# Kernel optimization log

Measured on AMD Instinct MI355X. Metric: run time of the kernel, lower is better.

Reference implementation:

```python
import jax, jax.numpy as jnp
import numpy as np

B, N, C, H = 1, 4096, 512, 8
S = 64  # sqrt(N), static


def setup_inputs() -> dict:
    key = jax.random.key(0)
    ks = jax.random.split(key, 4)
    d = C // H
    return {
        "x": jax.random.normal(ks[0], (B, N, C), dtype=jnp.float32),
        "num_heads": H,
        "bias": jnp.zeros((1,), dtype=jnp.float32),  # unused in original forward
        "scale": jnp.asarray(d ** -0.5, dtype=jnp.float32),
        "Wqkv": jax.random.normal(ks[1], (3 * C, C), dtype=jnp.float32) * (C ** -0.5),
        "bqkv": jnp.zeros((3 * C,), dtype=jnp.float32),
        "Wproj": jax.random.normal(ks[2], (C, C), dtype=jnp.float32) * (C ** -0.5),
        "bproj": jnp.zeros((C,), dtype=jnp.float32),
    }


def reference(x, num_heads, bias, scale, Wqkv, bqkv, Wproj, bproj):
    b, n, c = x.shape
    d = c // num_heads
    # fused QKV projection: [b, n, 3c] -> [3, b, h, n, d]
    qkv = (x @ Wqkv.T + bqkv).reshape(b, n, 3, num_heads, d).transpose(2, 0, 3, 1, 4)
    q, k, v = qkv[0] * scale, qkv[1], qkv[2]
    attn = jax.nn.softmax(jnp.einsum("bhnd,bhmd->bhnm", q, k), axis=-1)
    out = jnp.einsum("bhnm,bhmd->bhnd", attn, v)
    out = out.transpose(0, 2, 1, 3).reshape(b, n, c)
    out = out @ Wproj.T + bproj
    return out.reshape(b, S, S, c)
```

## Files before the change

### kernel.cpp

```cpp
#include <hip/hip_runtime.h>
#include <stdint.h>

#define NTOK 4096
#define CDIM 512
#define HEADS 8
#define DHEAD 64
#define PHEAD (NTOK * DHEAD)

typedef __bf16 bf16x8 __attribute__((ext_vector_type(8)));
typedef float f32x4 __attribute__((ext_vector_type(4)));

typedef const __attribute__((address_space(1))) unsigned int* gas_ptr;
typedef __attribute__((address_space(3))) unsigned int* las_ptr;

__device__ __forceinline__ unsigned short bfbits(float f) {
    return __builtin_bit_cast(unsigned short, (__bf16)f);
}

__device__ __forceinline__ f32x4 mfma32(bf16x8 a, bf16x8 b, f32x4 c) {
    return __builtin_amdgcn_mfma_f32_16x16x32_bf16(a, b, c, 0, 0, 0);
}

__device__ __forceinline__ void gload16(const unsigned short* g, unsigned short* l) {
    __builtin_amdgcn_global_load_lds((gas_ptr)g, (las_ptr)l, 16, 0, 0);
}

__device__ __forceinline__ void cvt_store8(unsigned short* dst, float4 v0, float4 v1) {
    unsigned short o[8];
    o[0] = bfbits(v0.x); o[1] = bfbits(v0.y); o[2] = bfbits(v0.z); o[3] = bfbits(v0.w);
    o[4] = bfbits(v1.x); o[5] = bfbits(v1.y); o[6] = bfbits(v1.z); o[7] = bfbits(v1.w);
    *(uint4*)dst = *(const uint4*)o;
}

__global__ __launch_bounds__(256) void cast3_k(
    const float* __restrict__ x, const float* __restrict__ wq, const float* __restrict__ wp,
    unsigned short* __restrict__ xb, unsigned short* __restrict__ wqb,
    unsigned short* __restrict__ wpb)
{
    const int b = blockIdx.x;
    const float* src; unsigned short* dst; int off;
    if (b < 1024)      { src = x;  dst = xb;  off = b; }
    else if (b < 1408) { src = wq; dst = wqb; off = b - 1024; }
    else               { src = wp; dst = wpb; off = b - 1408; }
    const int i = (off * 256 + threadIdx.x) * 8;
    const float4 v0 = *(const float4*)(src + i);
    const float4 v1 = *(const float4*)(src + i + 4);
    cvt_store8(dst + i, v0, v1);
}

__global__ __launch_bounds__(256) void gemm_qkv(
    const unsigned short* __restrict__ A,
    const unsigned short* __restrict__ Bm,
    const float* __restrict__ bias,
    const float* __restrict__ scale_p,
    unsigned short* __restrict__ qkv_out)
{
    __shared__ __align__(16) unsigned short smem[2 * 6144];

    const int tid = threadIdx.x;
    const int mBase = blockIdx.y * 64, nBase = blockIdx.x * 128;
    const int lane = tid & 63;
    const int w = __builtin_amdgcn_readfirstlane(tid >> 6);
    const int l16 = lane & 15, quad = lane >> 4;

    const int srow = tid >> 2;
    const int scol = ((tid & 3) ^ ((tid >> 3) & 3)) * 8;
    const unsigned short* gA  = &A[(size_t)(mBase + srow) * CDIM + scol];
    const unsigned short* gB0 = &Bm[(size_t)(nBase + srow) * CDIM + scol];
    const unsigned short* gB1 = &Bm[(size_t)(nBase + 64 + srow) * CDIM + scol];

    const int qs = (quad ^ ((l16 >> 1) & 3)) * 8;

    f32x4 acc[4][2] = {};

    gload16(gA, &smem[tid * 8]);
    gload16(gB0, &smem[2048 + tid * 8]);
    gload16(gB1, &smem[4096 + tid * 8]);

    int cur = 0;
    for (int kt = 0; kt < CDIM; kt += 32) {
        __syncthreads();
        if (kt + 32 < CDIM) {
            const int nb = (cur ^ 1) * 6144;
            gload16(gA + kt + 32, &smem[nb + tid * 8]);
            gload16(gB0 + kt + 32, &smem[nb + 2048 + tid * 8]);
            gload16(gB1 + kt + 32, &smem[nb + 4096 + tid * 8]);
        }
        const unsigned short* lA = &smem[cur * 6144];
        const unsigned short* lB = &smem[cur * 6144 + 2048];

        bf16x8 af[4], bfr[2];
#pragma unroll
        for (int i = 0; i < 4; ++i)
            af[i] = *(const bf16x8*)&lA[(i * 16 + l16) * 32 + qs];
#pragma unroll
        for (int j = 0; j < 2; ++j)
            bfr[j] = *(const bf16x8*)&lB[(w * 32 + j * 16 + l16) * 32 + qs];
#pragma unroll
        for (int i = 0; i < 4; ++i)
#pragma unroll
            for (int j = 0; j < 2; ++j)
                acc[i][j] = mfma32(af[i], bfr[j], acc[i][j]);
        cur ^= 1;
    }

    const int three = nBase >> 9;
    const float scl = scale_p[0] * 1.44269504f;
    const float mul = (three == 0) ? scl : 1.0f;

    __syncthreads();
#pragma unroll
    for (int i = 0; i < 4; ++i)
#pragma unroll
        for (int j = 0; j < 2; ++j)
#pragma unroll
            for (int r = 0; r < 4; ++r) {
                const int rl = i * 16 + quad * 4 + r;
                const int cl = w * 32 + j * 16 + l16;
                const float v = (acc[i][j][r] + bias[nBase + cl]) * mul;
                smem[rl * 136 + cl] = bfbits(v);
            }
    __syncthreads();

    const size_t base3 = (size_t)three * (PHEAD * HEADS);
    if (three < 2) {
#pragma unroll
        for (int pass = 0; pass < 4; ++pass) {
            const int idx = pass * 256 + tid;
            const int rl16 = idx & 15, qc = (idx >> 4) & 7;
            const int hsel = (idx >> 7) & 1, t16l = (idx >> 8) & 3;
            const uint4 d = *(const uint4*)&smem[(t16l * 16 + rl16) * 136 + hsel * 64 + qc * 8];
            const int hh = ((nBase >> 6) + hsel) & 7;
            const int t16 = (mBase >> 4) + t16l;
            const size_t dst = base3 + (size_t)hh * PHEAD +
                (size_t)(((t16 * 2 + (qc >> 2)) * 64 + (qc & 3) * 16 + rl16) * 8);
            *(uint4*)&qkv_out[dst] = d;
        }
    } else {
#pragma unroll
        for (int pass = 0; pass < 4; ++pass) {
            const int idx = pass * 256 + tid;
            const int l16t = idx & 15, quadt = (idx >> 4) & 3;
            const int dt = (idx >> 6) & 3, k32l = (idx >> 8) & 1, hsel = (idx >> 9) & 1;
            const int col = hsel * 64 + dt * 16 + l16t;
            unsigned short o8[8];
#pragma unroll
            for (int e = 0; e < 4; ++e) {
                o8[e]     = smem[(k32l * 32 + quadt * 4 + e) * 136 + col];
                o8[e + 4] = smem[(k32l * 32 + 16 + quadt * 4 + e) * 136 + col];
            }
            const int hh = ((nBase >> 6) + hsel) & 7;
            const int k32 = (mBase >> 5) + k32l;
            const size_t dst = base3 + (size_t)hh * PHEAD +
                (size_t)(((k32 * 4 + dt) * 64 + quadt * 16 + l16t) * 8);
            *(uint4*)&qkv_out[dst] = *(uint4*)o8;
        }
    }
}

__global__ __launch_bounds__(256, 2) void flash8_k(
    const unsigned short* __restrict__ qf,
    const unsigned short* __restrict__ kf,
    const unsigned short* __restrict__ vf,
    unsigned short* __restrict__ attn_out)
{
    __shared__ float ldsO[4][64][68];
    __shared__ float sml[4][64];

    const int tid = threadIdx.x;
    const int lane = tid & 63;
    const int w = __builtin_amdgcn_readfirstlane(tid >> 6);
    const int l16 = lane & 15, quad = lane >> 4;
    const int h = blockIdx.x, qb = blockIdx.y;

    const unsigned short* qh = qf + (size_t)h * PHEAD;
    const unsigned short* kb = kf + (size_t)h * PHEAD + w * 65536;
    const unsigned short* vb = vf + (size_t)h * PHEAD + w * 65536;

    bf16x8 qfr[4][2];
#pragma unroll
    for (int qt = 0; qt < 4; ++qt)
#pragma unroll
        for (int d2 = 0; d2 < 2; ++d2)
            qfr[qt][d2] = *(const bf16x8*)&qh[((qb * 4 + qt) * 2 + d2) * 512 + lane * 8];

    f32x4 oacc[4][4] = {};
    float lv[4] = {};

    bf16x8 kA[4], kB[4], vA[4], vB[4];
#pragma unroll
    for (int i = 0; i < 4; ++i) {
        kA[i] = *(const bf16x8*)&kb[i * 512 + lane * 8];
        vA[i] = *(const bf16x8*)&vb[i * 512 + lane * 8];
    }

    auto body = [&](int g, bf16x8* kuse, bf16x8* kload, bf16x8* vuse, bf16x8* vload) {
        const int gn = (g + 1) & 31;
#pragma unroll
        for (int i = 0; i < 4; ++i)
            kload[i] = *(const bf16x8*)&kb[gn * 2048 + i * 512 + lane * 8];
#pragma unroll
        for (int i = 0; i < 4; ++i)
            vload[i] = *(const bf16x8*)&vb[gn * 2048 + i * 512 + lane * 8];

        f32x4 s0[4], s1[4];
        __builtin_amdgcn_s_setprio(1);
#pragma unroll
        for (int qt = 0; qt < 4; ++qt) {
            f32x4 a = {};
            a = mfma32(kuse[0], qfr[qt][0], a);
            a = mfma32(kuse[1], qfr[qt][1], a);
            s0[qt] = a;
            f32x4 b = {};
            b = mfma32(kuse[2], qfr[qt][0], b);
            b = mfma32(kuse[3], qfr[qt][1], b);
            s1[qt] = b;
        }
        __builtin_amdgcn_s_setprio(0);

        bf16x8 pf[4];
#pragma unroll
        for (int qt = 0; qt < 4; ++qt) {
            float e0[4], e1[4];
#pragma unroll
            for (int r = 0; r < 4; ++r) {
                e0[r] = __builtin_amdgcn_exp2f(s0[qt][r]);
                e1[r] = __builtin_amdgcn_exp2f(s1[qt][r]);
            }
            lv[qt] += ((e0[0] + e0[1]) + (e0[2] + e0[3])) +
                      ((e1[0] + e1[1]) + (e1[2] + e1[3]));
            bf16x8 pb;
#pragma unroll
            for (int r = 0; r < 4; ++r) {
                pb[r]     = (__bf16)e0[r];
                pb[4 + r] = (__bf16)e1[r];
            }
            pf[qt] = pb;
        }

        __builtin_amdgcn_s_setprio(1);
#pragma unroll
        for (int dt = 0; dt < 4; ++dt)
#pragma unroll
            for (int qt = 0; qt < 4; ++qt)
                oacc[dt][qt] = mfma32(vuse[dt], pf[qt], oacc[dt][qt]);
        __builtin_amdgcn_s_setprio(0);
    };

    for (int it = 0; it < 16; ++it) {
        body(it * 2 + 0, kA, kB, vA, vB);
        body(it * 2 + 1, kB, kA, vB, vA);
    }

#pragma unroll
    for (int qt = 0; qt < 4; ++qt) {
        float L = lv[qt];
        L += __shfl_xor(L, 16, 64);
        L += __shfl_xor(L, 32, 64);
        if (quad == 0) sml[w][qt * 16 + l16] = L;
    }
#pragma unroll
    for (int qt = 0; qt < 4; ++qt) {
        const int q = qt * 16 + l16;
#pragma unroll
        for (int dt = 0; dt < 4; ++dt)
            *(f32x4*)&ldsO[w][q][dt * 16 + quad * 4] = oacc[dt][qt];
    }
    __syncthreads();
#pragma unroll
    for (int pass = 0; pass < 2; ++pass) {
        const int idx = pass * 256 + tid;
        const int q = idx >> 3, dseg = (idx & 7) * 8;
        const float L = sml[0][q] + sml[1][q] + sml[2][q] + sml[3][q];
        const float inv = 1.f / L;
        unsigned short o8[8];
#pragma unroll
        for (int i = 0; i < 8; ++i) {
            const float v = ldsO[0][q][dseg + i] + ldsO[1][q][dseg + i] +
                            ldsO[2][q][dseg + i] + ldsO[3][q][dseg + i];
            o8[i] = bfbits(v * inv);
        }
        *(uint4*)&attn_out[(size_t)(qb * 64 + q) * CDIM + h * DHEAD + dseg] = *(uint4*)o8;
    }
}

__global__ __launch_bounds__(256) void gemm_proj(
    const unsigned short* __restrict__ A,
    const unsigned short* __restrict__ Bm,
    const float* __restrict__ bias,
    float* __restrict__ c_out)
{
    __shared__ __align__(16) unsigned short smem[2 * 4096];

    const int tid = threadIdx.x;
    const int mBase = blockIdx.y * 64, nBase = blockIdx.x * 64;
    const int lane = tid & 63;
    const int w = __builtin_amdgcn_readfirstlane(tid >> 6);
    const int l16 = lane & 15, quad = lane >> 4;

    const int srow = tid >> 2;
    const int scol = ((tid & 3) ^ ((tid >> 3) & 3)) * 8;
    const unsigned short* gA = &A[(size_t)(mBase + srow) * CDIM + scol];
    const unsigned short* gB = &Bm[(size_t)(nBase + srow) * CDIM + scol];

    const int qs = (quad ^ ((l16 >> 1) & 3)) * 8;

    f32x4 acc[4] = {};

    gload16(gA, &smem[tid * 8]);
    gload16(gB, &smem[2048 + tid * 8]);

    int cur = 0;
    for (int kt = 0; kt < CDIM; kt += 32) {
        __syncthreads();
        if (kt + 32 < CDIM) {
            const int nb = (cur ^ 1) * 4096;
            gload16(gA + kt + 32, &smem[nb + tid * 8]);
            gload16(gB + kt + 32, &smem[nb + 2048 + tid * 8]);
        }
        const unsigned short* lA = &smem[cur * 4096];
        const unsigned short* lB = &smem[cur * 4096 + 2048];

        bf16x8 af[4], bfr;
#pragma unroll
        for (int i = 0; i < 4; ++i)
            af[i] = *(const bf16x8*)&lA[(i * 16 + l16) * 32 + qs];
        bfr = *(const bf16x8*)&lB[(w * 16 + l16) * 32 + qs];
#pragma unroll
        for (int i = 0; i < 4; ++i)
            acc[i] = mfma32(af[i], bfr, acc[i]);
        cur ^= 1;
    }

#pragma unroll
    for (int i = 0; i < 4; ++i)
#pragma unroll
        for (int r = 0; r < 4; ++r) {
            const int grow = mBase + i * 16 + quad * 4 + r;
            const int gcol = nBase + w * 16 + l16;
            c_out[(size_t)grow * CDIM + gcol] = acc[i][r] + bias[gcol];
        }
}

extern "C" void kernel_launch(void* const* d_in, const int* in_sizes, int n_in,
                              void* d_out, int out_size, void* d_ws, size_t ws_size,
                              hipStream_t stream) {
    const float* x       = (const float*)d_in[0];
    const float* scale_p = (const float*)d_in[3];
    const float* Wqkv    = (const float*)d_in[4];
    const float* bqkv    = (const float*)d_in[5];
    const float* Wproj   = (const float*)d_in[6];
    const float* bproj   = (const float*)d_in[7];
    float* out = (float*)d_out;

    char* ws = (char*)d_ws;
    const size_t OFF_QKV  = 0;
    const size_t OFF_ATTN = 12582912;
    const size_t OFF_XB   = 16777216;
    const size_t OFF_WQB  = 20971520;
    const size_t OFF_WPB  = 22544384;
    const size_t NEEDED   = OFF_WPB + 524288;
    if (ws_size < NEEDED) return;

    unsigned short* qkvb  = (unsigned short*)(ws + OFF_QKV);
    unsigned short* attnb = (unsigned short*)(ws + OFF_ATTN);
    unsigned short* xb    = (unsigned short*)(ws + OFF_XB);
    unsigned short* wqb   = (unsigned short*)(ws + OFF_WQB);
    unsigned short* wpb   = (unsigned short*)(ws + OFF_WPB);

    cast3_k<<<1536, 256, 0, stream>>>(x, Wqkv, Wproj, xb, wqb, wpb);

    gemm_qkv<<<dim3(12, 64), 256, 0, stream>>>(xb, wqb, bqkv, scale_p, qkvb);

    const unsigned short* qfr = qkvb;
    const unsigned short* kfr = qkvb + (size_t)PHEAD * HEADS;
    const unsigned short* vfr = qkvb + (size_t)2 * PHEAD * HEADS;
    flash8_k<<<dim3(8, 64), 256, 0, stream>>>(qfr, kfr, vfr, attnb);

    gemm_proj<<<dim3(8, 64), 256, 0, stream>>>(attnb, wpb, bproj, out);
}
```

Baseline: 131.4 us.

## Stage K/V tiles through LDS with async global-to-LDS double buffering

The attention kernel stops prefetching K and V into register double buffers and instead copies each tile into a double-buffered LDS region with global_load_lds. Each iteration then reads its fragments back from LDS, with a block barrier per iteration. The output-reduction epilogue now reuses the same 64KB buffer and works in two 32-row halves so everything fits. The aim is to lower register pressure and let the async copies hide load latency, at the cost of a barrier every iteration and extra LDS traffic.

Result: slower. 137.0 us (+4.2%).

```diff
diff --git a/kernel.cpp b/kernel.cpp
--- a/kernel.cpp
+++ b/kernel.cpp
@@ -158,14 +158,13 @@
     }
 }
 
-__global__ __launch_bounds__(256, 2) void flash8_k(
+__global__ __launch_bounds__(256, 2) void flash13_k(
     const unsigned short* __restrict__ qf,
     const unsigned short* __restrict__ kf,
     const unsigned short* __restrict__ vf,
     unsigned short* __restrict__ attn_out)
 {
-    __shared__ float ldsO[4][64][68];
-    __shared__ float sml[4][64];
+    __shared__ __align__(16) char sbuf[65536];
 
     const int tid = threadIdx.x;
     const int lane = tid & 63;
@@ -187,33 +186,40 @@
     f32x4 oacc[4][4] = {};
     float lv[4] = {};
 
-    bf16x8 kA[4], kB[4], vA[4], vB[4];
-#pragma unroll
-    for (int i = 0; i < 4; ++i) {
-        kA[i] = *(const bf16x8*)&kb[i * 512 + lane * 8];
-        vA[i] = *(const bf16x8*)&vb[i * 512 + lane * 8];
-    }
-
-    auto body = [&](int g, bf16x8* kuse, bf16x8* kload, bf16x8* vuse, bf16x8* vload) {
-        const int gn = (g + 1) & 31;
-#pragma unroll
-        for (int i = 0; i < 4; ++i)
-            kload[i] = *(const bf16x8*)&kb[gn * 2048 + i * 512 + lane * 8];
-#pragma unroll
-        for (int i = 0; i < 4; ++i)
-            vload[i] = *(const bf16x8*)&vb[gn * 2048 + i * 512 + lane * 8];
+    unsigned short* stg = (unsigned short*)sbuf + w * 4096;
+
+    auto STAGE = [&](int b, int g) {
+        unsigned short* s = stg + b * 16384;
+#pragma unroll
+        for (int i = 0; i < 4; ++i) {
+            gload16(&kb[g * 2048 + i * 512 + lane * 8], &s[i * 512 + lane * 8]);
+            gload16(&vb[g * 2048 + i * 512 + lane * 8], &s[2048 + i * 512 + lane * 8]);
+        }
+    };
+
+    STAGE(0, 0);
+    int cur = 0;
+    for (int g = 0; g < 32; ++g) {
+        __syncthreads();
+        if (g + 1 < 32) STAGE(cur ^ 1, g + 1);
+        const unsigned short* s = stg + cur * 16384;
+
+        bf16x8 kk[4];
+#pragma unroll
+        for (int i = 0; i < 4; ++i)
+            kk[i] = *(const bf16x8*)&s[i * 512 + lane * 8];
 
         f32x4 s0[4], s1[4];
         __builtin_amdgcn_s_setprio(1);
 #pragma unroll
         for (int qt = 0; qt < 4; ++qt) {
             f32x4 a = {};
-            a = mfma32(kuse[0], qfr[qt][0], a);
-            a = mfma32(kuse[1], qfr[qt][1], a);
+            a = mfma32(kk[0], qfr[qt][0], a);
+            a = mfma32(kk[1], qfr[qt][1], a);
             s0[qt] = a;
             f32x4 b = {};
-            b = mfma32(kuse[2], qfr[qt][0], b);
-            b = mfma32(kuse[3], qfr[qt][1], b);
+            b = mfma32(kk[2], qfr[qt][0], b);
+            b = mfma32(kk[3], qfr[qt][1], b);
             s1[qt] = b;
         }
         __builtin_amdgcn_s_setprio(0);
@@ -238,19 +244,25 @@
             pf[qt] = pb;
         }
 
+        bf16x8 vv[4];
+#pragma unroll
+        for (int i = 0; i < 4; ++i)
+            vv[i] = *(const bf16x8*)&s[2048 + i * 512 + lane * 8];
+
         __builtin_amdgcn_s_setprio(1);
 #pragma unroll
         for (int dt = 0; dt < 4; ++dt)
 #pragma unroll
             for (int qt = 0; qt < 4; ++qt)
-                oacc[dt][qt] = mfma32(vuse[dt], pf[qt], oacc[dt][qt]);
+                oacc[dt][qt] = mfma32(vv[dt], pf[qt], oacc[dt][qt]);
         __builtin_amdgcn_s_setprio(0);
-    };
-
-    for (int it = 0; it < 16; ++it) {
-        body(it * 2 + 0, kA, kB, vA, vB);
-        body(it * 2 + 1, kB, kA, vB, vA);
-    }
+        cur ^= 1;
+    }
+
+    __syncthreads();
+
+    float (*ldsO)[32][68] = (float(*)[32][68])sbuf;
+    float (*sml)[64]      = (float(*)[64])(sbuf + 34816);
 
 #pragma unroll
     for (int qt = 0; qt < 4; ++qt) {
@@ -259,28 +271,33 @@
         L += __shfl_xor(L, 32, 64);
         if (quad == 0) sml[w][qt * 16 + l16] = L;
     }
-#pragma unroll
-    for (int qt = 0; qt < 4; ++qt) {
-        const int q = qt * 16 + l16;
-#pragma unroll
-        for (int dt = 0; dt < 4; ++dt)
-            *(f32x4*)&ldsO[w][q][dt * 16 + quad * 4] = oacc[dt][qt];
-    }
-    __syncthreads();
-#pragma unroll
-    for (int pass = 0; pass < 2; ++pass) {
-        const int idx = pass * 256 + tid;
-        const int q = idx >> 3, dseg = (idx & 7) * 8;
-        const float L = sml[0][q] + sml[1][q] + sml[2][q] + sml[3][q];
-        const float inv = 1.f / L;
-        unsigned short o8[8];
-#pragma unroll
-        for (int i = 0; i < 8; ++i) {
-            const float v = ldsO[0][q][dseg + i] + ldsO[1][q][dseg + i] +
-                            ldsO[2][q][dseg + i] + ldsO[3][q][dseg + i];
-            o8[i] = bfbits(v * inv);
-        }
-        *(uint4*)&attn_out[(size_t)(qb * 64 + q) * CDIM + h * DHEAD + dseg] = *(uint4*)o8;
+
+#pragma unroll
+    for (int c = 0; c < 2; ++c) {
+#pragma unroll
+        for (int qh2 = 0; qh2 < 2; ++qh2) {
+            const int qt = c * 2 + qh2;
+            const int qrow = qh2 * 16 + l16;
+#pragma unroll
+            for (int dt = 0; dt < 4; ++dt)
+                *(f32x4*)&ldsO[w][qrow][dt * 16 + quad * 4] = oacc[dt][qt];
+        }
+        __syncthreads();
+        {
+            const int ql = tid >> 3, dseg = (tid & 7) * 8;
+            const int q = c * 32 + ql;
+            const float L = sml[0][q] + sml[1][q] + sml[2][q] + sml[3][q];
+            const float inv = 1.f / L;
+            unsigned short o8[8];
+#pragma unroll
+            for (int i = 0; i < 8; ++i) {
+                const float v = ldsO[0][ql][dseg + i] + ldsO[1][ql][dseg + i] +
+                                ldsO[2][ql][dseg + i] + ldsO[3][ql][dseg + i];
+                o8[i] = bfbits(v * inv);
+            }
+            *(uint4*)&attn_out[(size_t)(qb * 64 + q) * CDIM + h * DHEAD + dseg] = *(uint4*)o8;
+        }
+        __syncthreads();
     }
 }
 
@@ -375,7 +392,7 @@
     const unsigned short* qfr = qkvb;
     const unsigned short* kfr = qkvb + (size_t)PHEAD * HEADS;
     const unsigned short* vfr = qkvb + (size_t)2 * PHEAD * HEADS;
-    flash8_k<<<dim3(8, 64), 256, 0, stream>>>(qfr, kfr, vfr, attnb);
+    flash13_k<<<dim3(8, 64), 256, 0, stream>>>(qfr, kfr, vfr, attnb);
 
     gemm_proj<<<dim3(8, 64), 256, 0, stream>>>(attnb, wpb, bproj, out);
 }
```
